# Kernel tuning notes

Hardware: AMD Instinct MI355X
Metric: run time of the kernel (lower is better)

## Reference

```python
import jax, jax.numpy as jnp
import numpy as np


def setup_inputs() -> dict:
    key = jax.random.key(0)
    kq, kk, kv, kl = jax.random.split(key, 4)
    B, Nq, Nkv, D = 16, 2048, 2048, 64
    return {
        "Q_batch": jax.random.normal(kq, (B, Nq, D), dtype=jnp.float32),
        "K_batch": jax.random.normal(kk, (B, Nkv, D), dtype=jnp.float32),
        "V_batch": jax.random.normal(kv, (B, Nkv, D), dtype=jnp.float32),
        "valid_lens": jax.random.randint(kl, (B,), 0, Nkv, dtype=jnp.int64 if jax.config.jax_enable_x64 else jnp.int32),
    }


def reference(Q_batch, K_batch, V_batch, valid_lens):
    # S: (B, Nq, Nkv) scaled dot-product scores
    d = Q_batch.shape[-1]
    scale = 1.0 / jnp.sqrt(jnp.asarray(d, Q_batch.dtype))
    S = jnp.einsum('bqd,bkd->bqk', Q_batch, K_batch) * scale
    # mask_first_n_valid: position k valid iff k < valid_lens[b], broadcast over queries
    kv_idx = jnp.arange(S.shape[-1])  # (Nkv,)
    mask = kv_idx[None, None, :] < valid_lens[:, None, None]  # (B, 1->Nq, Nkv)
    S = jnp.where(mask, S, jnp.asarray(-1e20, S.dtype))
    W = jax.nn.softmax(S, axis=-1)  # attention weights (dropout rate = 0.0)
    return jnp.einsum('bqk,bkv->bqv', W, V_batch)
```

## Files before the change

### kernel.cpp

```cpp
#include <hip/hip_runtime.h>

#define BATCH 16
#define NQ    2048
#define NKV   2048
#define DH    64
#define SC    0.18033688011112042f
#define TILE_B 8192

typedef __attribute__((ext_vector_type(8))) short  bf16x8;
typedef __attribute__((ext_vector_type(16))) float f32x16;

__device__ __forceinline__ unsigned f2bf(float f) {
  unsigned u = __builtin_bit_cast(unsigned, f);
  u += 0x7FFFu + ((u >> 16) & 1u);
  return u >> 16;
}

__global__ __launch_bounds__(256) void convert_kernel(
    const float* __restrict__ K, const float* __restrict__ V,
    const int* __restrict__ lens, unsigned char* __restrict__ WS) {
  const int bt = blockIdx.x;
  const int b = bt >> 6, t = bt & 63;
  const int L = lens[b];
  const int Leff = (L == 0) ? NKV : L;
  if (t * 32 >= Leff) return;

  unsigned char* tile = WS + (size_t)bt * TILE_B;
  const size_t   srow = ((size_t)b * NKV + (size_t)t * 32) * DH;
  const int tid = threadIdx.x;
  const int l = tid & 63, g = tid >> 6;
  const int l31 = l & 31, hi = l >> 5;
  {
    const float4* p = (const float4*)(K + srow + (size_t)l31 * DH + g * 16 + hi * 8);
    float4 a = p[0], c4 = p[1];
    bf16x8 w;
    w[0] = (short)f2bf(a.x);  w[1] = (short)f2bf(a.y);
    w[2] = (short)f2bf(a.z);  w[3] = (short)f2bf(a.w);
    w[4] = (short)f2bf(c4.x); w[5] = (short)f2bf(c4.y);
    w[6] = (short)f2bf(c4.z); w[7] = (short)f2bf(c4.w);
    *(bf16x8*)(tile + g * 1024 + l * 16) = w;
  }
  {
    const int c2 = g & 1, dh = g >> 1;
    const float* vp = V + srow + (size_t)(c2 * 16 + 4 * hi) * DH + dh * 32 + l31;
    bf16x8 w;
#pragma unroll
    for (int j = 0; j < 8; ++j)
      w[j] = (short)f2bf(vp[(size_t)((j & 3) + 8 * (j >> 2)) * DH]);
    *(bf16x8*)(tile + 4096 + g * 1024 + l * 16) = w;
  }
}

__global__ __launch_bounds__(256, 3) void sdpa_kernel(
    const float* __restrict__ Q, const unsigned char* __restrict__ WS,
    const int* __restrict__ lens, float* __restrict__ O) {
  __shared__ float smem[6336];

  const int tid  = threadIdx.x;
  const int lane = tid & 63;
  const int wave = tid >> 6;
  const int l31  = lane & 31, hi = lane >> 5;

  const int idx = blockIdx.x, layer = idx >> 8, rr = idx & 255;
  const int b   = (rr + layer * 3) & 15;
  const int qo  = (rr >> 4) + layer * 16;

  const int  L    = lens[b];
  const bool zlen = (L == 0);
  const int  Leff = zlen ? NKV : L;
  const int  nT   = (Leff + 31) >> 5;
  const int  tb   = (nT * wave) >> 2;
  const int  cnt  = ((nT * (wave + 1)) >> 2) - tb;
  const int  tmask = (!zlen && (L & 31)) ? nT - 1 : -1;

  bf16x8 Qf[4];
  {
    const float* qp = Q + ((size_t)b * NQ + qo * 32 + l31) * DH + hi * 8;
#pragma unroll
    for (int c = 0; c < 4; ++c) {
      const float4* p = (const float4*)(qp + c * 16);
      float4 a = p[0], d4 = p[1];
      bf16x8 w;
      w[0] = (short)f2bf(a.x * SC);  w[1] = (short)f2bf(a.y * SC);
      w[2] = (short)f2bf(a.z * SC);  w[3] = (short)f2bf(a.w * SC);
      w[4] = (short)f2bf(d4.x * SC); w[5] = (short)f2bf(d4.y * SC);
      w[6] = (short)f2bf(d4.z * SC); w[7] = (short)f2bf(d4.w * SC);
      Qf[c] = w;
    }
  }

  const unsigned char* gp = WS + (size_t)(b * 64 + tb) * TILE_B + lane * 16;

  f32x16 oc0, oc1;
  float  l_ = 0.f;
#pragma unroll
  for (int r = 0; r < 16; ++r) { oc0[r] = 0.f; oc1[r] = 0.f; }

  bf16x8 cur[8];
  if (cnt > 0) {
#pragma unroll
    for (int i = 0; i < 8; ++i) cur[i] = *(const bf16x8*)(gp + i * 1024);
  }

  for (int it = 0; it < cnt; ++it) {
    const int t = tb + it;
    const unsigned char* gn = (it + 1 < cnt) ? (gp + TILE_B) : gp;
    bf16x8 nxt[8];
#pragma unroll
    for (int i = 0; i < 8; ++i) nxt[i] = *(const bf16x8*)(gn + i * 1024);
    gp += TILE_B;

    f32x16 acc;
#pragma unroll
    for (int r = 0; r < 16; ++r) acc[r] = 0.f;
#pragma unroll
    for (int c = 0; c < 4; ++c)
      acc = __builtin_amdgcn_mfma_f32_32x32x16_bf16(cur[c], Qf[c], acc, 0, 0, 0);

    if (zlen) {
#pragma unroll
      for (int r = 0; r < 16; ++r) acc[r] = 0.f;
    } else if (t == tmask) {
#pragma unroll
      for (int r = 0; r < 16; ++r) {
        const int key = t * 32 + (r & 3) + 8 * (r >> 2) + 4 * hi;
        if (key >= L) acc[r] = -1e30f;
      }
    }

    unsigned short ph[16];
    float ls = 0.f;
#pragma unroll
    for (int r = 0; r < 16; ++r) {
      float    p  = __builtin_amdgcn_exp2f(acc[r]);
      unsigned uu = __builtin_bit_cast(unsigned, p);
      ls += __builtin_bit_cast(float, uu & 0xFFFF0000u);
      ph[r] = (unsigned short)(uu >> 16);
    }
    l_ += ls;

    bf16x8 Pf0, Pf1;
#pragma unroll
    for (int j = 0; j < 8; ++j) { Pf0[j] = (short)ph[j]; Pf1[j] = (short)ph[8 + j]; }

    oc0 = __builtin_amdgcn_mfma_f32_32x32x16_bf16(cur[4], Pf0, oc0, 0, 0, 0);
    oc0 = __builtin_amdgcn_mfma_f32_32x32x16_bf16(cur[5], Pf1, oc0, 0, 0, 0);
    oc1 = __builtin_amdgcn_mfma_f32_32x32x16_bf16(cur[6], Pf0, oc1, 0, 0, 0);
    oc1 = __builtin_amdgcn_mfma_f32_32x32x16_bf16(cur[7], Pf1, oc1, 0, 0, 0);

#pragma unroll
    for (int i = 0; i < 8; ++i) cur[i] = nxt[i];
  }

  if (wave >= 1) {
    float* Mb = smem + (wave - 1) * 2112 + lane;
#pragma unroll
    for (int r = 0; r < 16; ++r) { Mb[r * 64] = oc0[r]; Mb[(16 + r) * 64] = oc1[r]; }
    Mb[32 * 64] = l_;
  }
  __syncthreads();
  if (wave == 0) {
#pragma unroll
    for (int w = 0; w < 3; ++w) {
      const float* Mb = smem + w * 2112 + lane;
#pragma unroll
      for (int r = 0; r < 16; ++r) { oc0[r] += Mb[r * 64]; oc1[r] += Mb[(16 + r) * 64]; }
      l_ += Mb[32 * 64];
    }
    const float inv = 1.0f / (l_ + __shfl_xor(l_, 32, 64));
#pragma unroll
    for (int r = 0; r < 16; ++r) {
      const int d0 = (r & 3) + 8 * (r >> 2) + 4 * hi;
      smem[l31 * 68 + d0]      = oc0[r] * inv;
      smem[l31 * 68 + 32 + d0] = oc1[r] * inv;
    }
  }
  __syncthreads();

  float* Ob = O + ((size_t)b * NQ + (size_t)qo * 32) * DH;
#pragma unroll
  for (int R = 0; R < 2; ++R) {
    const int fi = R * 256 + tid;
    const int q = fi >> 4, ch = fi & 15;
    float4 v4 = *(const float4*)&smem[q * 68 + ch * 4];
    *(float4*)(Ob + (size_t)q * DH + ch * 4) = v4;
  }
}

extern "C" void kernel_launch(void* const* d_in, const int* in_sizes, int n_in,
                              void* d_out, int out_size, void* d_ws, size_t ws_size,
                              hipStream_t stream) {
  const float* Q    = (const float*)d_in[0];
  const float* K    = (const float*)d_in[1];
  const float* V    = (const float*)d_in[2];
  const int*   lens = (const int*)d_in[3];
  float*       Out  = (float*)d_out;
  unsigned char* WS = (unsigned char*)d_ws;

  hipLaunchKernelGGL(convert_kernel, dim3(BATCH * 64), dim3(256), 0, stream, K, V, lens, WS);
  hipLaunchKernelGGL(sdpa_kernel, dim3(1024), dim3(256), 0, stream, Q, WS, lens, Out);
}
```

Baseline: 97.96 us.

## Read fp32 K directly in attention kernel, pre-convert only V

The pre-pass now converts only V to bf16 tiles, with one wave per tile and fewer blocks. The attention kernel loads K as fp32 straight from global memory, converts it in registers with packed bf16 conversions, and prefetches the next tile. A zero-length batch is now handled by scaling Q by zero rather than zeroing scores. This removes the K workspace write and reread and shrinks the convert launch, at the cost of twice the K bytes loaded per attention block and extra conversion ALU work inside the main loop.

```diff
diff --git a/kernel.cpp b/kernel.cpp
--- a/kernel.cpp
+++ b/kernel.cpp
@@ -1,11 +1,12 @@
 #include <hip/hip_runtime.h>
+#include <hip/hip_bf16.h>
 
 #define BATCH 16
 #define NQ    2048
 #define NKV   2048
 #define DH    64
 #define SC    0.18033688011112042f
-#define TILE_B 8192
+#define VTILE_B 4096
 
 typedef __attribute__((ext_vector_type(8))) short  bf16x8;
 typedef __attribute__((ext_vector_type(16))) float f32x16;
@@ -16,44 +17,36 @@
   return u >> 16;
 }
 
-__global__ __launch_bounds__(256) void convert_kernel(
-    const float* __restrict__ K, const float* __restrict__ V,
-    const int* __restrict__ lens, unsigned char* __restrict__ WS) {
-  const int bt = blockIdx.x;
-  const int b = bt >> 6, t = bt & 63;
-  const int L = lens[b];
+__global__ __launch_bounds__(256) void convert_v(
+    const float* __restrict__ V, const int* __restrict__ lens,
+    unsigned char* __restrict__ WS) {
+  const int tid  = threadIdx.x;
+  const int wave = tid >> 6, l = tid & 63;
+  const int b    = blockIdx.x >> 4;
+  const int t    = (blockIdx.x & 15) * 4 + wave;
+  const int L    = lens[b];
   const int Leff = (L == 0) ? NKV : L;
   if (t * 32 >= Leff) return;
 
-  unsigned char* tile = WS + (size_t)bt * TILE_B;
+  unsigned char* tile = WS + (size_t)(b * 64 + t) * VTILE_B;
   const size_t   srow = ((size_t)b * NKV + (size_t)t * 32) * DH;
-  const int tid = threadIdx.x;
-  const int l = tid & 63, g = tid >> 6;
   const int l31 = l & 31, hi = l >> 5;
-  {
-    const float4* p = (const float4*)(K + srow + (size_t)l31 * DH + g * 16 + hi * 8);
-    float4 a = p[0], c4 = p[1];
-    bf16x8 w;
-    w[0] = (short)f2bf(a.x);  w[1] = (short)f2bf(a.y);
-    w[2] = (short)f2bf(a.z);  w[3] = (short)f2bf(a.w);
-    w[4] = (short)f2bf(c4.x); w[5] = (short)f2bf(c4.y);
-    w[6] = (short)f2bf(c4.z); w[7] = (short)f2bf(c4.w);
-    *(bf16x8*)(tile + g * 1024 + l * 16) = w;
-  }
-  {
+#pragma unroll
+  for (int g = 0; g < 4; ++g) {
     const int c2 = g & 1, dh = g >> 1;
     const float* vp = V + srow + (size_t)(c2 * 16 + 4 * hi) * DH + dh * 32 + l31;
     bf16x8 w;
 #pragma unroll
     for (int j = 0; j < 8; ++j)
       w[j] = (short)f2bf(vp[(size_t)((j & 3) + 8 * (j >> 2)) * DH]);
-    *(bf16x8*)(tile + 4096 + g * 1024 + l * 16) = w;
+    *(bf16x8*)(tile + g * 1024 + l * 16) = w;
   }
 }
 
 __global__ __launch_bounds__(256, 3) void sdpa_kernel(
-    const float* __restrict__ Q, const unsigned char* __restrict__ WS,
-    const int* __restrict__ lens, float* __restrict__ O) {
+    const float* __restrict__ Q, const float* __restrict__ K,
+    const unsigned char* __restrict__ WS, const int* __restrict__ lens,
+    float* __restrict__ O) {
   __shared__ float smem[6336];
 
   const int tid  = threadIdx.x;
@@ -75,52 +68,84 @@
 
   bf16x8 Qf[4];
   {
+    const float sc = zlen ? 0.f : SC;
     const float* qp = Q + ((size_t)b * NQ + qo * 32 + l31) * DH + hi * 8;
 #pragma unroll
     for (int c = 0; c < 4; ++c) {
       const float4* p = (const float4*)(qp + c * 16);
       float4 a = p[0], d4 = p[1];
       bf16x8 w;
-      w[0] = (short)f2bf(a.x * SC);  w[1] = (short)f2bf(a.y * SC);
-      w[2] = (short)f2bf(a.z * SC);  w[3] = (short)f2bf(a.w * SC);
-      w[4] = (short)f2bf(d4.x * SC); w[5] = (short)f2bf(d4.y * SC);
-      w[6] = (short)f2bf(d4.z * SC); w[7] = (short)f2bf(d4.w * SC);
+      w[0] = (short)f2bf(a.x * sc);  w[1] = (short)f2bf(a.y * sc);
+      w[2] = (short)f2bf(a.z * sc);  w[3] = (short)f2bf(a.w * sc);
+      w[4] = (short)f2bf(d4.x * sc); w[5] = (short)f2bf(d4.y * sc);
+      w[6] = (short)f2bf(d4.z * sc); w[7] = (short)f2bf(d4.w * sc);
       Qf[c] = w;
     }
   }
 
-  const unsigned char* gp = WS + (size_t)(b * 64 + tb) * TILE_B + lane * 16;
+  const float* kp = K + ((size_t)b * NKV + (size_t)tb * 32 + l31) * DH + hi * 8;
+  const unsigned char* gv = WS + (size_t)(b * 64 + tb) * VTILE_B + lane * 16;
 
   f32x16 oc0, oc1;
   float  l_ = 0.f;
 #pragma unroll
   for (int r = 0; r < 16; ++r) { oc0[r] = 0.f; oc1[r] = 0.f; }
 
-  bf16x8 cur[8];
+  float4 Kr[8];
+  bf16x8 Vn[4];
   if (cnt > 0) {
 #pragma unroll
-    for (int i = 0; i < 8; ++i) cur[i] = *(const bf16x8*)(gp + i * 1024);
+    for (int c = 0; c < 4; ++c) {
+      Kr[2 * c]     = *(const float4*)(kp + c * 16);
+      Kr[2 * c + 1] = *(const float4*)(kp + c * 16 + 4);
+    }
+#pragma unroll
+    for (int i = 0; i < 4; ++i) Vn[i] = *(const bf16x8*)(gv + i * 1024);
   }
 
   for (int it = 0; it < cnt; ++it) {
     const int t = tb + it;
-    const unsigned char* gn = (it + 1 < cnt) ? (gp + TILE_B) : gp;
-    bf16x8 nxt[8];
-#pragma unroll
-    for (int i = 0; i < 8; ++i) nxt[i] = *(const bf16x8*)(gn + i * 1024);
-    gp += TILE_B;
+
+    bf16x8 cK[4];
+#pragma unroll
+    for (int c = 0; c < 4; ++c) {
+      const float4 a = Kr[2 * c], d4 = Kr[2 * c + 1];
+      __hip_bfloat162 p0 = __float22bfloat162_rn({a.x, a.y});
+      __hip_bfloat162 p1 = __float22bfloat162_rn({a.z, a.w});
+      __hip_bfloat162 p2 = __float22bfloat162_rn({d4.x, d4.y});
+      __hip_bfloat162 p3 = __float22bfloat162_rn({d4.z, d4.w});
+      bf16x8 w;
+      w[0] = __builtin_bit_cast(short, p0.x); w[1] = __builtin_bit_cast(short, p0.y);
+      w[2] = __builtin_bit_cast(short, p1.x); w[3] = __builtin_bit_cast(short, p1.y);
+      w[4] = __builtin_bit_cast(short, p2.x); w[5] = __builtin_bit_cast(short, p2.y);
+      w[6] = __builtin_bit_cast(short, p3.x); w[7] = __builtin_bit_cast(short, p3.y);
+      cK[c] = w;
+    }
 
     f32x16 acc;
 #pragma unroll
     for (int r = 0; r < 16; ++r) acc[r] = 0.f;
 #pragma unroll
     for (int c = 0; c < 4; ++c)
-      acc = __builtin_amdgcn_mfma_f32_32x32x16_bf16(cur[c], Qf[c], acc, 0, 0, 0);
-
-    if (zlen) {
-#pragma unroll
-      for (int r = 0; r < 16; ++r) acc[r] = 0.f;
-    } else if (t == tmask) {
+      acc = __builtin_amdgcn_mfma_f32_32x32x16_bf16(cK[c], Qf[c], acc, 0, 0, 0);
+
+    bf16x8 cV[4];
+#pragma unroll
+    for (int i = 0; i < 4; ++i) cV[i] = Vn[i];
+    {
+      const bool more = (it + 1 < cnt);
+      const float*         kn = more ? (kp + (size_t)(it + 1) * 32 * DH) : (kp + (size_t)it * 32 * DH);
+      const unsigned char* vn = more ? (gv + (size_t)(it + 1) * VTILE_B) : (gv + (size_t)it * VTILE_B);
+#pragma unroll
+      for (int c = 0; c < 4; ++c) {
+        Kr[2 * c]     = *(const float4*)(kn + c * 16);
+        Kr[2 * c + 1] = *(const float4*)(kn + c * 16 + 4);
+      }
+#pragma unroll
+      for (int i = 0; i < 4; ++i) Vn[i] = *(const bf16x8*)(vn + i * 1024);
+    }
+
+    if (t == tmask) {
 #pragma unroll
       for (int r = 0; r < 16; ++r) {
         const int key = t * 32 + (r & 3) + 8 * (r >> 2) + 4 * hi;
@@ -143,13 +168,10 @@
 #pragma unroll
     for (int j = 0; j < 8; ++j) { Pf0[j] = (short)ph[j]; Pf1[j] = (short)ph[8 + j]; }
 
-    oc0 = __builtin_amdgcn_mfma_f32_32x32x16_bf16(cur[4], Pf0, oc0, 0, 0, 0);
-    oc0 = __builtin_amdgcn_mfma_f32_32x32x16_bf16(cur[5], Pf1, oc0, 0, 0, 0);
-    oc1 = __builtin_amdgcn_mfma_f32_32x32x16_bf16(cur[6], Pf0, oc1, 0, 0, 0);
-    oc1 = __builtin_amdgcn_mfma_f32_32x32x16_bf16(cur[7], Pf1, oc1, 0, 0, 0);
-
-#pragma unroll
-    for (int i = 0; i < 8; ++i) cur[i] = nxt[i];
+    oc0 = __builtin_amdgcn_mfma_f32_32x32x16_bf16(cV[0], Pf0, oc0, 0, 0, 0);
+    oc0 = __builtin_amdgcn_mfma_f32_32x32x16_bf16(cV[1], Pf1, oc0, 0, 0, 0);
+    oc1 = __builtin_amdgcn_mfma_f32_32x32x16_bf16(cV[2], Pf0, oc1, 0, 0, 0);
+    oc1 = __builtin_amdgcn_mfma_f32_32x32x16_bf16(cV[3], Pf1, oc1, 0, 0, 0);
   }
 
   if (wave >= 1) {
@@ -197,6 +219,6 @@
   float*       Out  = (float*)d_out;
   unsigned char* WS = (unsigned char*)d_ws;
 
-  hipLaunchKernelGGL(convert_kernel, dim3(BATCH * 64), dim3(256), 0, stream, K, V, lens, WS);
-  hipLaunchKernelGGL(sdpa_kernel, dim3(1024), dim3(256), 0, stream, Q, WS, lens, Out);
-}
+  hipLaunchKernelGGL(convert_v, dim3(BATCH * 16), dim3(256), 0, stream, V, lens, WS);
+  hipLaunchKernelGGL(sdpa_kernel, dim3(1024), dim3(256), 0, stream, Q, K, WS, lens, Out);
+}
```

Result: slower. 132.9 us (+35.7%).
